# Optimization experiments

Measured on AMD Instinct MI355X. Metric: run time of the kernel, lower is better.

The kernel has to match this reference:

```python
import jax, jax.numpy as jnp
import numpy as np

TOP_K = 8
N_EXPERTS = 256
N_GROUP = 8
TOPK_GROUP = 4
ROUTED_SCALING = 2.5
NORM_TOPK_PROB = True
HIDDEN = 4096
TOKENS = 16384


def setup_inputs() -> dict:
    key = jax.random.key(0)
    k1, k2, k3 = jax.random.split(key, 3)
    hidden_states = jax.random.normal(k1, (TOKENS, HIDDEN), dtype=jnp.float32)
    weight = jax.random.normal(k2, (N_EXPERTS, HIDDEN), dtype=jnp.float32) * 0.02
    e_score_correction_bias = jax.random.normal(k3, (N_EXPERTS,), dtype=jnp.float32) * 0.1
    return {
        "hidden_states": hidden_states,
        "weight": weight,
        "e_score_correction_bias": e_score_correction_bias,
    }


def _get_topk_indices(scores, bias):
    # scores: [T, E]
    T = scores.shape[0]
    scores_for_choice = scores + bias[None, :]                      # [T, E]
    grp = scores_for_choice.reshape(T, N_GROUP, N_EXPERTS // N_GROUP)
    top2_vals, _ = jax.lax.top_k(grp, 2)                            # [T, G, 2]
    group_scores = top2_vals.sum(axis=-1)                           # [T, G]
    _, group_idx = jax.lax.top_k(group_scores, TOPK_GROUP)          # [T, topk_group]
    group_mask = jnp.zeros((T, N_GROUP), dtype=scores.dtype)
    group_mask = jnp.take_along_axis(group_mask, group_idx, axis=1)  # placeholder, replaced below
    # scatter 1s into selected groups
    group_mask = jnp.zeros((T, N_GROUP), dtype=bool)
    group_mask = group_mask.at[jnp.arange(T)[:, None], group_idx].set(True)
    score_mask = jnp.repeat(group_mask, N_EXPERTS // N_GROUP, axis=1)  # [T, E]
    masked = jnp.where(score_mask, scores_for_choice, 0.0)
    _, topk_indices = jax.lax.top_k(masked, TOP_K)                  # [T, top_k]
    return topk_indices


def reference(hidden_states, weight, e_score_correction_bias):
    # router logits: [T, E]
    router_logits = jnp.einsum("th,eh->te", hidden_states.astype(jnp.float32),
                               weight.astype(jnp.float32))
    scores = jax.nn.sigmoid(router_logits)
    topk_indices = _get_topk_indices(scores, e_score_correction_bias)
    topk_weights = jnp.take_along_axis(scores, topk_indices, axis=1)  # [T, top_k]
    if NORM_TOPK_PROB:
        denom = topk_weights.sum(axis=-1, keepdims=True) + 1e-20
        topk_weights = topk_weights / denom
    topk_weights = topk_weights * ROUTED_SCALING
    return topk_indices, topk_weights.astype(jnp.float32)
```

## Files before the change

### kernel.cpp

```cpp
#include <hip/hip_runtime.h>
#include <math.h>

#define T_TOKENS 16384
#define HID      4096
#define NEXP     256
#define NGROUP   8
#define GSIZE    32
#define TOPKG    4
#define TOPK     8
#define RSCALE   2.5f

#define TAU   1.5e-5f
#define TAUG  2.5e-5f

#define BM     64
#define BK     32
#define SPLITK 4
#define KSPAN  (HID / SPLITK)
#define NKS    (KSPAN / BK)
#define NSG    (HID / BK)

#define A_HI   0
#define A_LO   2048
#define A_TOT  4096

#define WQ_LIMB (NSG * 8192)

#define RT_TOK 16

typedef __attribute__((ext_vector_type(8))) short bf16x8;
typedef __attribute__((ext_vector_type(4))) float f32x4;

__device__ __forceinline__ int stoffA(int r, int q) {
    return (r >> 4) * 512 + (q >> 1) * 128 + (r & 15) * 8 + (q & 1) * 4;
}
__device__ __forceinline__ int froffL(int lane) {
    return (lane >> 4) * 128 + (lane & 15) * 8;
}

__device__ __forceinline__ void split4(const float4 v, uint& h01, uint& h23,
                                       uint& l01, uint& l23) {
    const uint u0 = __float_as_uint(v.x) + 0x8000u;
    const uint u1 = __float_as_uint(v.y) + 0x8000u;
    const uint u2 = __float_as_uint(v.z) + 0x8000u;
    const uint u3 = __float_as_uint(v.w) + 0x8000u;
    h01 = __builtin_amdgcn_perm(u1, u0, 0x07060302u);
    h23 = __builtin_amdgcn_perm(u3, u2, 0x07060302u);
    const float f0 = v.x - __uint_as_float(u0 & 0xFFFF0000u);
    const float f1 = v.y - __uint_as_float(u1 & 0xFFFF0000u);
    const float f2 = v.z - __uint_as_float(u2 & 0xFFFF0000u);
    const float f3 = v.w - __uint_as_float(u3 & 0xFFFF0000u);
    l01 = __builtin_amdgcn_perm(__float_as_uint(f1) + 0x8000u,
                                __float_as_uint(f0) + 0x8000u, 0x07060302u);
    l23 = __builtin_amdgcn_perm(__float_as_uint(f3) + 0x8000u,
                                __float_as_uint(f2) + 0x8000u, 0x07060302u);
}

template <class SC>
__device__ __forceinline__ bool route_core(SC sc, const float* __restrict__ bias,
                                           int* id, float* wv)
{
    float gs[NGROUP];
#pragma unroll
    for (int g = 0; g < NGROUP; ++g) {
        float m1 = -1e30f, m2 = -1e30f;
        for (int i = 0; i < GSIZE; ++i) {
            const int e = g * GSIZE + i;
            const float v = sc(e) + bias[e];
            if (v > m1)      { m2 = m1; m1 = v; }
            else if (v > m2) { m2 = v; }
        }
        gs[g] = m1 + m2;
    }

    unsigned gmask = 0;
    float g4 = -1e30f;
#pragma unroll
    for (int r = 0; r < TOPKG; ++r) {
        int bi = 0; float bv = -1e30f;
#pragma unroll
        for (int g = 0; g < NGROUP; ++g) {
            const bool taken = (gmask >> g) & 1;
            if (!taken && gs[g] > bv) { bv = gs[g]; bi = g; }
        }
        gmask |= 1u << bi;
        g4 = bv;
    }
    float g5 = -1e30f;
#pragma unroll
    for (int g = 0; g < NGROUP; ++g)
        if (!((gmask >> g) & 1) && gs[g] > g5) g5 = gs[g];

    float val[TOPK + 1]; int vid[TOPK + 1];
#pragma unroll
    for (int r = 0; r <= TOPK; ++r) { val[r] = -1e30f; vid[r] = 0; }
    for (int e = 0; e < NEXP; ++e) {
        const bool allowed = (gmask >> (e >> 5)) & 1;
        const float v = allowed ? (sc(e) + bias[e]) : 0.0f;
        if (v > val[TOPK]) {
#pragma unroll
            for (int p = TOPK; p >= 1; --p) {
                if (v > val[p - 1])  { val[p] = val[p - 1]; vid[p] = vid[p - 1]; }
                else if (v > val[p]) { val[p] = v;          vid[p] = e; }
            }
            if (v > val[0]) { val[0] = v; vid[0] = e; }
        }
    }

    bool tight = (g4 - g5 < TAUG);
#pragma unroll
    for (int i = 0; i < TOPK; ++i) tight |= (val[i] - val[i + 1] < TAU);

    float sum = 0.0f;
#pragma unroll
    for (int r = 0; r < TOPK; ++r) { id[r] = vid[r]; wv[r] = sc(vid[r]); sum += wv[r]; }
    const float inv = RSCALE / (sum + 1e-20f);
#pragma unroll
    for (int r = 0; r < TOPK; ++r) wv[r] *= inv;
    return tight;
}

__device__ void exact_token(const float* __restrict__ hs, const float* __restrict__ wt,
                            const float* __restrict__ bias, float* __restrict__ out, int t)
{
    float lg[NEXP];
    const float* hrow = hs + (size_t)t * HID;
    for (int e = 0; e < NEXP; ++e) {
        const float* wr = wt + (size_t)e * HID;
        float a = 0.0f;
        for (int k = 0; k < HID; k += 4) {
            const float4 x = *(const float4*)(hrow + k);
            const float4 b = *(const float4*)(wr + k);
            a = fmaf(x.x, b.x, a); a = fmaf(x.y, b.y, a);
            a = fmaf(x.z, b.z, a); a = fmaf(x.w, b.w, a);
        }
        lg[e] = 1.0f / (1.0f + expf(-a));
    }
    int id[TOPK]; float wv[TOPK];
    route_core([&](int e) { return lg[e]; }, bias, id, wv);
    for (int r = 0; r < TOPK; ++r) {
        out[(size_t)t * TOPK + r] = (float)id[r];
        out[(size_t)T_TOKENS * TOPK + (size_t)t * TOPK + r] = wv[r];
    }
}

__global__ __launch_bounds__(256, 8)
void conv_weight(const float* __restrict__ wt, ushort* __restrict__ wq)
{
    const int g  = blockIdx.x * 256 + threadIdx.x;
    const int e  = g >> 9;
    const int kc = g & 511;
    const int sg  = kc >> 2;
    const int kch = kc & 3;

    const float4 v0 = *(const float4*)(wt + (size_t)e * HID + kc * 8);
    const float4 v1 = *(const float4*)(wt + (size_t)e * HID + kc * 8 + 4);
    uint h01, h23, l01, l23, h45, h67, l45, l67;
    split4(v0, h01, h23, l01, l23);
    split4(v1, h45, h67, l45, l67);

    const size_t idx = (size_t)sg * 8192 + (size_t)((e >> 4) * 512 + kch * 128 + (e & 15) * 8);
    uint4 hv; hv.x = h01; hv.y = h23; hv.z = h45; hv.w = h67;
    uint4 lv; lv.x = l01; lv.y = l23; lv.z = l45; lv.w = l67;
    *(uint4*)&wq[idx] = hv;
    *(uint4*)&wq[(size_t)WQ_LIMB + idx] = lv;
}

__global__ __launch_bounds__(256, 4)
void router_gemm(const float* __restrict__ hs, const ushort* __restrict__ wq,
                 float* __restrict__ pw)
{
    __shared__ ushort u16[A_TOT];

    const int tid  = threadIdx.x;
    const int lane = tid & 63;
    const int w    = tid >> 6;
    const int b    = blockIdx.x;
    const int m    = (b >> 5) * 8 + (b & 7);
    const int sk   = (b >> 3) & 3;
    const int t0   = m * BM;
    const int kb0  = sk * KSPAN;
    const int r0   = tid >> 3;
    const int q    = tid & 7;

    const ushort* wq_hi = wq;
    const ushort* wq_lo = wq + WQ_LIMB;

    f32x4 acc[4][4];
#pragma unroll
    for (int i = 0; i < 4; ++i)
#pragma unroll
        for (int j = 0; j < 4; ++j) acc[i][j] = (f32x4)0.0f;

    float4 ra[2];
#pragma unroll
    for (int s = 0; s < 2; ++s)
        ra[s] = *(const float4*)(hs + (size_t)(t0 + r0 + 32 * s) * HID + kb0 + q * 4);

    for (int ks = 0; ks < NKS; ++ks) {
        const int sg = sk * NKS + ks;
        __syncthreads();

#pragma unroll
        for (int s = 0; s < 2; ++s) {
            const int r = r0 + 32 * s;
            uint h01, h23, l01, l23;
            split4(ra[s], h01, h23, l01, l23);
            const int eo = stoffA(r, q);
            uint2 hv; hv.x = h01; hv.y = h23;
            uint2 lv; lv.x = l01; lv.y = l23;
            *(uint2*)&u16[A_HI + eo] = hv;
            *(uint2*)&u16[A_LO + eo] = lv;
        }
        __syncthreads();

        bf16x8 bh[4], bl[4];
        {
            const size_t bb = (size_t)sg * 8192 + (size_t)(w * 4) * 512 + (size_t)lane * 8;
#pragma unroll
            for (int c = 0; c < 4; ++c) {
                bh[c] = *(const bf16x8*)(wq_hi + bb + c * 512);
                bl[c] = *(const bf16x8*)(wq_lo + bb + c * 512);
            }
        }
        if (ks + 1 < NKS) {
            const int kb = kb0 + (ks + 1) * BK;
#pragma unroll
            for (int s = 0; s < 2; ++s)
                ra[s] = *(const float4*)(hs + (size_t)(t0 + r0 + 32 * s) * HID + kb + q * 4);
        }

        const int fo = froffL(lane);
        bf16x8 ah[4], al[4];
#pragma unroll
        for (int rt = 0; rt < 4; ++rt) {
            ah[rt] = *(const bf16x8*)&u16[A_HI + rt * 512 + fo];
            al[rt] = *(const bf16x8*)&u16[A_LO + rt * 512 + fo];
        }
#pragma unroll
        for (int c = 0; c < 4; ++c) {
#pragma unroll
            for (int rt = 0; rt < 4; ++rt) {
                acc[rt][c] = __builtin_amdgcn_mfma_f32_16x16x32_bf16(ah[rt], bh[c], acc[rt][c], 0, 0, 0);
                acc[rt][c] = __builtin_amdgcn_mfma_f32_16x16x32_bf16(ah[rt], bl[c], acc[rt][c], 0, 0, 0);
                acc[rt][c] = __builtin_amdgcn_mfma_f32_16x16x32_bf16(al[rt], bh[c], acc[rt][c], 0, 0, 0);
            }
        }
    }

#pragma unroll
    for (int rt = 0; rt < 4; ++rt)
#pragma unroll
        for (int c = 0; c < 4; ++c) {
            const int col  = w * 64 + c * 16 + (lane & 15);
            const int rowb = rt * 16 + (lane >> 4) * 4;
#pragma unroll
            for (int j = 0; j < 4; ++j)
                pw[((size_t)(sk * T_TOKENS) + t0 + rowb + j) * NEXP + col] = acc[rt][c][j];
        }
}

__global__ __launch_bounds__(256, 4)
void router_route(const float* __restrict__ pw, const float* __restrict__ bias,
                  float* __restrict__ out,
                  unsigned* __restrict__ wcnt, unsigned* __restrict__ wlist,
                  unsigned cap)
{
    __shared__ float Lg[NEXP * RT_TOK];
    const int tid  = threadIdx.x;
    const int b    = blockIdx.x;
    const int x    = b & 7;
    const int rest = b >> 3;
    const int m    = (rest >> 2) * 8 + x;
    const int sub  = rest & 3;
    const int t0   = m * BM + sub * RT_TOK;

#pragma unroll
    for (int t = 0; t < RT_TOK; ++t) {
        float v = 0.0f;
#pragma unroll
        for (int s = 0; s < SPLITK; ++s)
            v += pw[((size_t)(s * T_TOKENS) + t0 + t) * NEXP + tid];
        Lg[tid * RT_TOK + ((t + tid) & (RT_TOK - 1))] = 1.0f / (1.0f + expf(-v));
    }
    __syncthreads();

    if (tid < RT_TOK) {
        const int t = t0 + tid;
        int id[TOPK]; float wv[TOPK];
        const bool tight = route_core(
            [&](int e) { return Lg[e * RT_TOK + ((tid + e) & (RT_TOK - 1))]; },
            bias, id, wv);

#pragma unroll
        for (int r = 0; r < TOPK; ++r) {
            out[(size_t)t * TOPK + r] = (float)id[r];
            out[(size_t)T_TOKENS * TOPK + (size_t)t * TOPK + r] = wv[r];
        }
        if (tight) {
            const unsigned pos = atomicAdd(wcnt, 1u);
            if (pos < cap) wlist[pos] = (unsigned)t;
        }
    }
}

__global__ __launch_bounds__(256, 4)
void router_exact(const float* __restrict__ hs, const float* __restrict__ wt,
                  const float* __restrict__ bias, float* __restrict__ out,
                  const unsigned* __restrict__ wcnt, const unsigned* __restrict__ wlist,
                  unsigned cap)
{
    __shared__ float hrow[HID];
    __shared__ float lg[NEXP];
    const unsigned count = min(*wcnt, cap);
    const int tid  = threadIdx.x;
    const int lane = tid & 63;
    const int w    = tid >> 6;

    for (unsigned b = blockIdx.x; b < count; b += gridDim.x) {
        __syncthreads();
        const int t = (int)wlist[b];

#pragma unroll
        for (int i = 0; i < 4; ++i) {
            const int f4 = i * 256 + tid;
            *(float4*)&hrow[f4 * 4] = *(const float4*)(hs + (size_t)t * HID + f4 * 4);
        }
        __syncthreads();

        for (int g = 0; g < 16; ++g) {
            const int e0 = w * 64 + g * 4;
            float a[4] = {0.0f, 0.0f, 0.0f, 0.0f};
#pragma unroll 4
            for (int j = 0; j < 16; ++j) {
                const int f4 = j * 64 + lane;
                const float4 h = *(const float4*)&hrow[f4 * 4];
#pragma unroll
                for (int p = 0; p < 4; ++p) {
                    const float4 v = *(const float4*)(wt + (size_t)(e0 + p) * HID + f4 * 4);
                    a[p] = fmaf(h.x, v.x, a[p]); a[p] = fmaf(h.y, v.y, a[p]);
                    a[p] = fmaf(h.z, v.z, a[p]); a[p] = fmaf(h.w, v.w, a[p]);
                }
            }
#pragma unroll
            for (int p = 0; p < 4; ++p)
#pragma unroll
                for (int d = 1; d < 64; d <<= 1)
                    a[p] += __shfl_xor(a[p], d, 64);
            if (lane == 0) {
#pragma unroll
                for (int p = 0; p < 4; ++p)
                    lg[e0 + p] = 1.0f / (1.0f + expf(-a[p]));
            }
        }
        __syncthreads();

        if (tid == 0) {
            int id[TOPK]; float wv[TOPK];
            route_core([&](int e) { return lg[e]; }, bias, id, wv);
            for (int r = 0; r < TOPK; ++r) {
                out[(size_t)t * TOPK + r] = (float)id[r];
                out[(size_t)T_TOKENS * TOPK + (size_t)t * TOPK + r] = wv[r];
            }
        }
    }
}

__global__ __launch_bounds__(512, 1)
void router_mono(const float* __restrict__ hs, const float* __restrict__ wt,
                 const float* __restrict__ bias, float* __restrict__ out,
                 unsigned* __restrict__ wcnt, unsigned* __restrict__ wlist, unsigned cap)
{
    __shared__ float smem[16384];
    ushort* u16 = (ushort*)smem;
    float*  Lg  = smem;

    const int tid  = threadIdx.x;
    const int lane = tid & 63;
    const int w    = tid >> 6;
    const int t0   = blockIdx.x * 64;
    const int ar   = tid >> 3;
    const int aq   = tid & 7;

    f32x4 acc[4][2];
#pragma unroll
    for (int i = 0; i < 4; ++i)
#pragma unroll
        for (int j = 0; j < 2; ++j) acc[i][j] = (f32x4)0.0f;

    float4 ra, rb[4];
    ra = *(const float4*)(hs + (size_t)(t0 + ar) * HID + aq * 4);
#pragma unroll
    for (int s = 0; s < 4; ++s)
        rb[s] = *(const float4*)(wt + (size_t)(ar + s * 64) * HID + aq * 4);

    for (int ks = 0; ks < HID / BK; ++ks) {
        __syncthreads();
        {
            uint h01, h23, l01, l23;
            split4(ra, h01, h23, l01, l23);
            const int eo = stoffA(ar, aq);
            uint2 hv; hv.x = h01; hv.y = h23;
            uint2 lv; lv.x = l01; lv.y = l23;
            *(uint2*)&u16[0 + eo] = hv;
            *(uint2*)&u16[2048 + eo] = lv;
        }
#pragma unroll
        for (int s = 0; s < 4; ++s) {
            const int e = ar + s * 64;
            uint h01, h23, l01, l23;
            split4(rb[s], h01, h23, l01, l23);
            const int eo = stoffA(e, aq);
            uint2 hv; hv.x = h01; hv.y = h23;
            uint2 lv; lv.x = l01; lv.y = l23;
            *(uint2*)&u16[4096 + eo] = hv;
            *(uint2*)&u16[12288 + eo] = lv;
        }
        __syncthreads();
        if (ks + 1 < HID / BK) {
            const int k0 = (ks + 1) * BK;
            ra = *(const float4*)(hs + (size_t)(t0 + ar) * HID + k0 + aq * 4);
#pragma unroll
            for (int s = 0; s < 4; ++s)
                rb[s] = *(const float4*)(wt + (size_t)(ar + s * 64) * HID + k0 + aq * 4);
        }
        const int fo = froffL(lane);
        bf16x8 ah[4], al[4];
#pragma unroll
        for (int rt = 0; rt < 4; ++rt) {
            ah[rt] = *(const bf16x8*)&u16[0 + rt * 512 + fo];
            al[rt] = *(const bf16x8*)&u16[2048 + rt * 512 + fo];
        }
#pragma unroll
        for (int c = 0; c < 2; ++c) {
            const int ct = w * 2 + c;
            const bf16x8 bh = *(const bf16x8*)&u16[4096 + ct * 512 + fo];
            const bf16x8 bl = *(const bf16x8*)&u16[12288 + ct * 512 + fo];
#pragma unroll
            for (int rt = 0; rt < 4; ++rt) {
                acc[rt][c] = __builtin_amdgcn_mfma_f32_16x16x32_bf16(ah[rt], bh, acc[rt][c], 0, 0, 0);
                acc[rt][c] = __builtin_amdgcn_mfma_f32_16x16x32_bf16(ah[rt], bl, acc[rt][c], 0, 0, 0);
                acc[rt][c] = __builtin_amdgcn_mfma_f32_16x16x32_bf16(al[rt], bh, acc[rt][c], 0, 0, 0);
            }
        }
    }
    __syncthreads();
#pragma unroll
    for (int rt = 0; rt < 4; ++rt)
#pragma unroll
        for (int c = 0; c < 2; ++c) {
            const int col  = w * 32 + c * 16 + (lane & 15);
            const int rowb = rt * 16 + (lane >> 4) * 4;
#pragma unroll
            for (int j = 0; j < 4; ++j) {
                const int row = rowb + j;
                Lg[col * 64 + ((row + col) & 63)] = 1.0f / (1.0f + expf(-acc[rt][c][j]));
            }
        }
    __syncthreads();

    if (tid < 64) {
        const int t = t0 + tid;
        int id[TOPK]; float wv[TOPK];
        const bool tight = route_core(
            [&](int e) { return Lg[e * 64 + ((tid + e) & 63)]; }, bias, id, wv);
#pragma unroll
        for (int r = 0; r < TOPK; ++r) {
            out[(size_t)t * TOPK + r] = (float)id[r];
            out[(size_t)T_TOKENS * TOPK + (size_t)t * TOPK + r] = wv[r];
        }
        if (tight) {
            bool queued = false;
            if (wcnt) {
                const unsigned pos = atomicAdd(wcnt, 1u);
                if (pos < cap) { wlist[pos] = (unsigned)t; queued = true; }
            }
            if (!queued) exact_token(hs, wt, bias, out, t);
        }
    }
}

extern "C" void kernel_launch(void* const* d_in, const int* in_sizes, int n_in,
                              void* d_out, int out_size, void* d_ws, size_t ws_size,
                              hipStream_t stream) {
    const float* hs   = (const float*)d_in[0];
    const float* wt   = (const float*)d_in[1];
    const float* bias = (const float*)d_in[2];
    float* out = (float*)d_out;
    (void)in_sizes; (void)n_in; (void)out_size;

    const size_t PW_BYTES = (size_t)SPLITK * T_TOKENS * NEXP * 4;
    const size_t WQ_BYTES = (size_t)2 * WQ_LIMB * 2;
    const size_t NEED = PW_BYTES + WQ_BYTES + 4 + (size_t)T_TOKENS * 4;

    if (ws_size >= NEED) {
        float*    pw    = (float*)d_ws;
        ushort*   wq    = (ushort*)((char*)d_ws + PW_BYTES);
        unsigned* wcnt  = (unsigned*)((char*)d_ws + PW_BYTES + WQ_BYTES);
        unsigned* wlist = wcnt + 1;
        hipMemsetAsync(wcnt, 0, sizeof(unsigned), stream);
        conv_weight<<<512, 256, 0, stream>>>(wt, wq);
        router_gemm<<<(T_TOKENS / BM) * SPLITK, 256, 0, stream>>>(hs, wq, pw);
        router_route<<<T_TOKENS / RT_TOK, 256, 0, stream>>>(pw, bias, out, wcnt, wlist,
                                                            (unsigned)T_TOKENS);
        router_exact<<<2048, 256, 0, stream>>>(hs, wt, bias, out, wcnt, wlist,
                                               (unsigned)T_TOKENS);
    } else if (ws_size >= 8) {
        unsigned cap = (unsigned)((ws_size - 4) / 4);
        if (cap > T_TOKENS) cap = T_TOKENS;
        unsigned* wcnt  = (unsigned*)d_ws;
        unsigned* wlist = wcnt + 1;
        hipMemsetAsync(d_ws, 0, sizeof(unsigned), stream);
        router_mono<<<T_TOKENS / 64, 512, 0, stream>>>(hs, wt, bias, out, wcnt, wlist, cap);
        router_exact<<<2048, 256, 0, stream>>>(hs, wt, bias, out, wcnt, wlist, cap);
    } else {
        router_mono<<<T_TOKENS / 64, 512, 0, stream>>>(hs, wt, bias, out,
                                                       nullptr, nullptr, 0u);
    }
}
```

Baseline: 330.0 us.

## Double-buffer A tile in LDS to cut one barrier per k-step

Converts the router GEMM's shared-memory A tile into a ping-pong double buffer. The next stage is split into bf16 limbs and written to the alternate buffer while the current one is read for MFMA. The global load is issued two stages ahead, which removes one of the two __syncthreads per k-step. This doubles LDS use per block (16 KB), which may affect occupancy, and keeps prefetched registers live longer.

```diff
diff --git a/kernel.cpp b/kernel.cpp
--- a/kernel.cpp
+++ b/kernel.cpp
@@ -22,7 +22,7 @@
 
 #define A_HI   0
 #define A_LO   2048
-#define A_TOT  4096
+#define A_BUF  4096
 
 #define WQ_LIMB (NSG * 8192)
 
@@ -170,7 +170,7 @@
 void router_gemm(const float* __restrict__ hs, const ushort* __restrict__ wq,
                  float* __restrict__ pw)
 {
-    __shared__ ushort u16[A_TOT];
+    __shared__ ushort u16[2 * A_BUF];
 
     const int tid  = threadIdx.x;
     const int lane = tid & 63;
@@ -193,26 +193,48 @@
         for (int j = 0; j < 4; ++j) acc[i][j] = (f32x4)0.0f;
 
     float4 ra[2];
-#pragma unroll
-    for (int s = 0; s < 2; ++s)
-        ra[s] = *(const float4*)(hs + (size_t)(t0 + r0 + 32 * s) * HID + kb0 + q * 4);
-
-    for (int ks = 0; ks < NKS; ++ks) {
-        const int sg = sk * NKS + ks;
-        __syncthreads();
-
+    {
 #pragma unroll
         for (int s = 0; s < 2; ++s) {
-            const int r = r0 + 32 * s;
+            const float4 v = *(const float4*)(hs + (size_t)(t0 + r0 + 32 * s) * HID + kb0 + q * 4);
             uint h01, h23, l01, l23;
-            split4(ra[s], h01, h23, l01, l23);
-            const int eo = stoffA(r, q);
+            split4(v, h01, h23, l01, l23);
+            const int eo = stoffA(r0 + 32 * s, q);
             uint2 hv; hv.x = h01; hv.y = h23;
             uint2 lv; lv.x = l01; lv.y = l23;
             *(uint2*)&u16[A_HI + eo] = hv;
             *(uint2*)&u16[A_LO + eo] = lv;
         }
-        __syncthreads();
+#pragma unroll
+        for (int s = 0; s < 2; ++s)
+            ra[s] = *(const float4*)(hs + (size_t)(t0 + r0 + 32 * s) * HID + kb0 + BK + q * 4);
+    }
+    __syncthreads();
+
+    int cur = 0;
+    for (int ks = 0; ks < NKS; ++ks) {
+        const int sg = sk * NKS + ks;
+        ushort* bc = u16 + cur * A_BUF;
+        ushort* bn = u16 + (cur ^ 1) * A_BUF;
+
+        if (ks + 1 < NKS) {
+#pragma unroll
+            for (int s = 0; s < 2; ++s) {
+                uint h01, h23, l01, l23;
+                split4(ra[s], h01, h23, l01, l23);
+                const int eo = stoffA(r0 + 32 * s, q);
+                uint2 hv; hv.x = h01; hv.y = h23;
+                uint2 lv; lv.x = l01; lv.y = l23;
+                *(uint2*)&bn[A_HI + eo] = hv;
+                *(uint2*)&bn[A_LO + eo] = lv;
+            }
+            if (ks + 2 < NKS) {
+                const int kb = kb0 + (ks + 2) * BK;
+#pragma unroll
+                for (int s = 0; s < 2; ++s)
+                    ra[s] = *(const float4*)(hs + (size_t)(t0 + r0 + 32 * s) * HID + kb + q * 4);
+            }
+        }
 
         bf16x8 bh[4], bl[4];
         {
@@ -223,19 +245,13 @@
                 bl[c] = *(const bf16x8*)(wq_lo + bb + c * 512);
             }
         }
-        if (ks + 1 < NKS) {
-            const int kb = kb0 + (ks + 1) * BK;
-#pragma unroll
-            for (int s = 0; s < 2; ++s)
-                ra[s] = *(const float4*)(hs + (size_t)(t0 + r0 + 32 * s) * HID + kb + q * 4);
-        }
 
         const int fo = froffL(lane);
         bf16x8 ah[4], al[4];
 #pragma unroll
         for (int rt = 0; rt < 4; ++rt) {
-            ah[rt] = *(const bf16x8*)&u16[A_HI + rt * 512 + fo];
-            al[rt] = *(const bf16x8*)&u16[A_LO + rt * 512 + fo];
+            ah[rt] = *(const bf16x8*)&bc[A_HI + rt * 512 + fo];
+            al[rt] = *(const bf16x8*)&bc[A_LO + rt * 512 + fo];
         }
 #pragma unroll
         for (int c = 0; c < 4; ++c) {
@@ -246,6 +262,9 @@
                 acc[rt][c] = __builtin_amdgcn_mfma_f32_16x16x32_bf16(al[rt], bh[c], acc[rt][c], 0, 0, 0);
             }
         }
+
+        __syncthreads();
+        cur ^= 1;
     }
 
 #pragma unroll
```

Measured after the change: 331.3 us. Within noise of the previous version (+0.4%).
